# Optimization experiments

Measured on AMD Instinct MI355X. Metric: run time of the kernel, lower is better.

Reference implementation:

```python
import jax, jax.numpy as jnp
import numpy as np
import math

B, N, D, KA, H = 8, 1024, 512, 16, 8
QD = D // 4
HD = D // H


def qsplit(x):
    q = x.shape[-1] // 4
    return x[..., :q], x[..., q:2*q], x[..., 2*q:3*q], x[..., 3*q:]


def hprod(p, q):
    pr, pi, pj, pk = qsplit(p)
    qr, qi, qj, qk = qsplit(q)
    return jnp.concatenate([
        pr*qr - pi*qi - pj*qj - pk*qk,
        pr*qi + pi*qr + pj*qk - pk*qj,
        pr*qj - pi*qk + pj*qr + pk*qi,
        pr*qk + pi*qj - pj*qi + pk*qr,
    ], axis=-1)


def qconj(x):
    r, i, j, k = qsplit(x)
    return jnp.concatenate([r, -i, -j, -k], axis=-1)


def qlin(x, w, b):
    # w: [4, qo, qi] -> Hamilton block matrix [4qo, 4qi]
    r, i, j, k = w[0], w[1], w[2], w[3]
    W = jnp.concatenate([
        jnp.concatenate([r, -i, -j, -k], axis=1),
        jnp.concatenate([i,  r, -k,  j], axis=1),
        jnp.concatenate([j,  k,  r, -i], axis=1),
        jnp.concatenate([k, -j,  i,  r], axis=1),
    ], axis=0)
    return x @ W.T + b


def qln(x, gamma, beta):
    # per-component LayerNorm over Q; gamma/beta: [4, Q]
    qd = x.shape[-1] // 4
    xs = x.reshape(x.shape[:-1] + (4, qd))
    m = xs.mean(-1, keepdims=True)
    v = xs.var(-1, keepdims=True)
    y = (xs - m) / jnp.sqrt(v + 1e-5) * gamma + beta
    return y.reshape(x.shape)


def setup_inputs():
    key = jax.random.key(0)
    ks = jax.random.split(key, 20)
    lim = math.sqrt(6.0 / (2 * QD))  # xavier for [QD, QD]
    def qw(k):
        return jax.random.uniform(k, (4, QD, QD), minval=-lim, maxval=lim)
    return {
        'q': jax.random.normal(ks[0], (B, N, D), dtype=jnp.float32),
        'spike': jax.random.uniform(ks[1], (B, N), dtype=jnp.float32),
        'mask': jnp.ones((B, N), dtype=jnp.float32),
        'theta_logit': jnp.float32(0.0),
        'w_prim': qw(ks[2]), 'b_prim': jnp.zeros((D,), jnp.float32),
        'anchors': jax.random.normal(ks[3], (KA, D)) * 0.5,
        'log_sigma': jnp.zeros((KA,), jnp.float32),
        'w_aggr': qw(ks[4]), 'b_aggr': jnp.zeros((D,), jnp.float32),
        'w_q': qw(ks[5]), 'b_q': jnp.zeros((D,), jnp.float32),
        'w_k': qw(ks[6]), 'b_k': jnp.zeros((D,), jnp.float32),
        'w_v': qw(ks[7]), 'b_v': jnp.zeros((D,), jnp.float32),
        'w_o': qw(ks[8]), 'b_o': jnp.zeros((D,), jnp.float32),
        'ln_gamma': jnp.ones((4, QD), jnp.float32),
        'ln_beta': jnp.zeros((4, QD), jnp.float32),
    }


def reference(q, spike, mask, theta_logit, w_prim, b_prim, anchors, log_sigma,
              w_aggr, b_aggr, w_q, b_q, w_k, b_k, w_v, b_v, w_o, b_o,
              ln_gamma, ln_beta):
    b, n, d = q.shape
    qd = d // 4
    # --- SpikeQuaternionRotation: rotate toward K-axis by theta = theta_max*spike ---
    theta_max = (jnp.pi / 2) * jax.nn.sigmoid(theta_logit)
    theta = theta_max * spike                      # [B, N]
    c = jnp.cos(theta)[..., None]
    s = jnp.sin(theta)[..., None]
    z = jnp.zeros_like(c)
    rot = jnp.concatenate([
        jnp.broadcast_to(c, (b, n, qd)),
        jnp.broadcast_to(z, (b, n, qd)),
        jnp.broadcast_to(z, (b, n, qd)),
        jnp.broadcast_to(s, (b, n, qd)),
    ], axis=-1)
    q_rot = hprod(rot, q)                          # [B, N, D]

    # --- PrimaryLayer: per-cell quaternion transform ---
    msg_p = qlin(q_rot, w_prim, b_prim)

    # --- QuaternionAnchorLayer ---
    a_conj = qconj(anchors)                        # [KA, D]
    prod = hprod(q_rot[:, None, :, :], a_conj[None, :, None, :])  # [B, KA, N, D]
    dist = jnp.sum(prod * prod, axis=-1)           # [B, KA, N]
    sigma_sq = jnp.maximum(jnp.exp(log_sigma) ** 2, 1e-6)
    incid = jnp.exp(-dist / sigma_sq[None, :, None]) * mask[:, None, :]
    denom = jnp.maximum(incid.sum(-1, keepdims=True), 1e-6)
    h = jnp.einsum('bkn,bnd->bkd', incid, q_rot) / denom  # [B, KA, D]
    h = qlin(h, w_aggr, b_aggr)

    # --- QuaternionMHA(query=q_rot, key=h, value=h), no mask ---
    Qh = qlin(q_rot, w_q, b_q).reshape(b, n, H, HD)
    Kh = qlin(h, w_k, b_k).reshape(b, KA, H, HD)
    Vh = qlin(h, w_v, b_v).reshape(b, KA, H, HD)
    scores = jnp.einsum('bqhd,bkhd->bhqk', Qh, Kh) / jnp.sqrt(jnp.float32(HD))
    attn = jax.nn.softmax(scores, axis=-1)
    out = jnp.einsum('bhqk,bkhd->bqhd', attn, Vh).reshape(b, n, d)
    msg_a = qlin(out, w_o, b_o)

    # --- residual + per-component LayerNorm ---
    return qln(q + msg_p + msg_a, ln_gamma, ln_beta)
```

## Files before the change

kernel.cpp:

```cpp
#include <hip/hip_runtime.h>
#include <hip/hip_bf16.h>

typedef __hip_bfloat16 bf16;
typedef __attribute__((ext_vector_type(8))) short bf16x8;
typedef __attribute__((ext_vector_type(4))) float f32x4;

__device__ __forceinline__ float bflo(unsigned u) { return __uint_as_float(u << 16); }
__device__ __forceinline__ float bfhi(unsigned u) { return __uint_as_float(u & 0xffff0000u); }
__device__ __forceinline__ bool probe_f32(const void* mask) {
  return *(const unsigned*)mask == 0x3F800000u;
}
__device__ __forceinline__ float ldin(const void* p, size_t i, bool f32) {
  return f32 ? ((const float*)p)[i] : (float)((const bf16*)p)[i];
}


__global__ __launch_bounds__(256) void prologue(
    const void* w0, const void* w1, const void* w2, const void* w3,
    const void* w4, const void* w5,
    const void* b0, const void* b1, const void* b2, const void* b3,
    const void* b4, const void* b5, const void* g_, const void* be,
    const void* q, const void* spike, const void* theta_logit, const void* mask,
    bf16* __restrict__ Wall, float* __restrict__ biasF,
    bf16* __restrict__ q_rot, float* __restrict__ qn) {
  bool f32 = probe_f32(mask);
  int blk = blockIdx.x, t = threadIdx.x;
  if (blk < 1536) {
    const int compT[4][4] = {{0,1,2,3},{1,0,3,2},{2,3,0,1},{3,2,1,0}};
    const float signT[4][4] = {{1.f,-1.f,-1.f,-1.f},{1.f,1.f,-1.f,1.f},{1.f,1.f,1.f,-1.f},{1.f,-1.f,1.f,1.f}};
    int E = blk * 1024 + t * 4;
    int g = E >> 9;
    int wi = g >> 9;
    int o = g & 511;
    int k0 = E & 511;
    const void* src = wi == 0 ? w0 : wi == 1 ? w1 : wi == 2 ? w2 : wi == 3 ? w3 : wi == 4 ? w4 : w5;
    int ro = o >> 7, a = o & 127, co = k0 >> 7;
    int comp = compT[ro][co];
    float sgn = signT[ro][co];
    bf16 ov[4];
    #pragma unroll
    for (int j = 0; j < 4; ++j) {
      int b2 = (k0 & 127) + j;
      ov[j] = (bf16)(ldin(src, comp * 16384 + a * 128 + b2, f32) * sgn);
    }
    int r = g & 63, c = k0 >> 3;
    size_t off = (size_t)(g >> 6) * 65536 + (size_t)((c >> 2) * 4096 + (r >> 4) * 1024
               + ((c & 3) * 16 + (r & 15)) * 16 + (k0 & 7) * 2);
    *(uint2*)((char*)Wall + off) = *(const uint2*)ov;
  } else if (blk < 1544) {
    int b = blk - 1536;
    const void* src = b == 0 ? b0 : b == 1 ? b1 : b == 2 ? b2 : b == 3 ? b3
                    : b == 4 ? b4 : b == 5 ? b5 : b == 6 ? g_ : be;
    biasF[b * 512 + t] = ldin(src, t, f32);
    biasF[b * 512 + 256 + t] = ldin(src, 256 + t, f32);
  } else {
    int row = (blk - 1544) * 2 + (t >> 7);
    int l = t & 127;
    float tl = ldin(theta_logit, 0, f32);
    float tmax = 1.5707963267948966f / (1.0f + __expf(-tl));
    float th = tmax * ldin(spike, row, f32);
    float c = cosf(th), s = sinf(th);
    size_t base = (size_t)row * 512;
    float a = ldin(q, base + l, f32), b = ldin(q, base + 128 + l, f32);
    float cc = ldin(q, base + 256 + l, f32), d = ldin(q, base + 384 + l, f32);
    float r0 = c * a - s * d;
    float r1 = c * b - s * cc;
    float r2 = c * cc + s * b;
    float r3 = c * d + s * a;
    bf16* orow = q_rot + base;
    orow[l] = (bf16)r0; orow[128 + l] = (bf16)r1; orow[256 + l] = (bf16)r2; orow[384 + l] = (bf16)r3;
    qn[(size_t)row * 128 + l] = r0 * r0 + r1 * r1 + r2 * r2 + r3 * r3;
  }
}

__device__ __forceinline__ void stage_B64(const bf16* __restrict__ Bw, int n0, char* Bs, int t) {
  const char* src = (const char*)Bw + (size_t)(n0 >> 6) * 65536;
  #pragma unroll
  for (int i = 0; i < 16; ++i)
    *(uint4*)(Bs + t * 16 + i * 4096) = *(const uint4*)(src + t * 16 + i * 4096);
}

__global__ __launch_bounds__(256, 2) void gemm_dist(
    const bf16* __restrict__ A, const bf16* __restrict__ Bw,
    const float* __restrict__ bias0, const float* __restrict__ bias1,
    bf16* __restrict__ MQ,
    const float* __restrict__ qn, const void* anchors, const void* lsig,
    const void* mask, float* __restrict__ h_part, float* __restrict__ pd_part) {
  __shared__ char smem[77952];
  const int t = threadIdx.x;
  if (blockIdx.x >= 128) {
    char* Bs = smem;
    const int g = blockIdx.x - 128;
    const int wave = t >> 6, lane = t & 63;
    const int quad = lane >> 4, l16 = lane & 15;
    const int m0 = (g & 31) * 256, n0 = (g >> 5) * 64;
    stage_B64(Bw, n0, Bs, t);
    __syncthreads();
    const int mbase = m0 + wave * 64;
    f32x4 acc[4][4] = {};
    bf16x8 areg[2][4], breg[2][4];
    #pragma unroll
    for (int mt = 0; mt < 4; ++mt)
      areg[0][mt] = *(const bf16x8*)(A + (size_t)(mbase + mt * 16 + l16) * 512 + quad * 8);
    #pragma unroll
    for (int nt = 0; nt < 4; ++nt)
      breg[0][nt] = *(const bf16x8*)(Bs + nt * 1024 + lane * 16);
    #pragma unroll
    for (int kk = 0; kk < 16; ++kk) {
      const int cur = kk & 1, nxt = cur ^ 1;
      if (kk < 15) {
        const int k2 = (kk + 1) * 32;
        #pragma unroll
        for (int mt = 0; mt < 4; ++mt)
          areg[nxt][mt] = *(const bf16x8*)(A + (size_t)(mbase + mt * 16 + l16) * 512 + k2 + quad * 8);
        #pragma unroll
        for (int nt = 0; nt < 4; ++nt)
          breg[nxt][nt] = *(const bf16x8*)(Bs + (kk + 1) * 4096 + nt * 1024 + lane * 16);
      }
      #pragma unroll
      for (int mt = 0; mt < 4; ++mt)
        #pragma unroll
        for (int nt = 0; nt < 4; ++nt)
          acc[mt][nt] = __builtin_amdgcn_mfma_f32_16x16x32_bf16(areg[cur][mt], breg[cur][nt],
                                                                acc[mt][nt], 0, 0, 0);
    }
    #pragma unroll
    for (int nt = 0; nt < 4; ++nt) {
      int col = n0 + nt * 16 + l16;
      float bv = col < 512 ? bias0[col] : bias1[col - 512];
      #pragma unroll
      for (int mt = 0; mt < 4; ++mt) {
        int rb = mbase + mt * 16 + quad * 4;
        #pragma unroll
        for (int r = 0; r < 4; ++r)
          MQ[(size_t)(rb + r) * 1024 + col] = (bf16)(acc[mt][nt][r] + bv);
      }
    }
  } else {
    bool f32 = probe_f32(mask);
    bf16*  qr   = (bf16*)smem;
    float* an   = (float*)(smem + 65536);
    float* sInc = (float*)(smem + 73728);
    float* rs   = (float*)(smem + 77824);
    float* pd   = (float*)(smem + 77888);
    int bb = blockIdx.x;
    int b = bb >> 4, nc = bb & 15;
    {
      const uint4* src = (const uint4*)((const bf16*)A + ((size_t)b * 1024 + nc * 64) * 512);
      uint4* dst = (uint4*)qr;
      #pragma unroll
      for (int i = 0; i < 16; ++i) dst[t + i * 256] = src[t + i * 256];
    }
    for (int i = t; i < 2048; i += 256) {
      int k = i >> 7, l = i & 127;
      float a0 = ldin(anchors, k * 512 + l, f32);
      float a1 = ldin(anchors, k * 512 + 128 + l, f32);
      float a2 = ldin(anchors, k * 512 + 256 + l, f32);
      float a3 = ldin(anchors, k * 512 + 384 + l, f32);
      an[i] = a0 * a0 + a1 * a1 + a2 * a2 + a3 * a3;
    }
    if (t < 16) {
      float ls = ldin(lsig, t, f32);
      float ssq = __expf(ls); ssq = fmaxf(ssq * ssq, 1e-6f);
      rs[t] = -1.0f / ssq;
      pd[t] = 0.0f;
    }
    __syncthreads();
    {
      int rl = t >> 2, part = t & 3;
      int n = nc * 64 + rl;
      const float* qrow = qn + ((size_t)b * 1024 + n) * 128 + part * 32;
      f32x4 q4[8];
      #pragma unroll
      for (int i = 0; i < 8; ++i) q4[i] = *(const f32x4*)(qrow + i * 4);
      float sc[16] = {};
      #pragma unroll
      for (int i = 0; i < 8; ++i) {
        #pragma unroll
        for (int k = 0; k < 16; ++k) {
          f32x4 av = *(const f32x4*)(an + k * 128 + part * 32 + i * 4);
          sc[k] += q4[i][0] * av[0] + q4[i][1] * av[1] + q4[i][2] * av[2] + q4[i][3] * av[3];
        }
      }
      #pragma unroll
      for (int k = 0; k < 16; ++k) {
        sc[k] += __shfl_xor(sc[k], 1, 64);
        sc[k] += __shfl_xor(sc[k], 2, 64);
      }
      if (part == 0) {
        float mval = ldin(mask, b * 1024 + n, f32);
        #pragma unroll
        for (int k = 0; k < 16; ++k) {
          float inc = __expf(sc[k] * rs[k]) * mval;
          sInc[k * 64 + rl] = inc;
          atomicAdd(&pd[k], inc);
        }
      }
    }
    __syncthreads();
    {
      float acc0[16] = {}, acc1[16] = {};
      for (int nn = 0; nn < 64; ++nn) {
        float v0 = (float)qr[nn * 512 + t];
        float v1 = (float)qr[nn * 512 + 256 + t];
        #pragma unroll
        for (int k = 0; k < 16; ++k) {
          float p = sInc[k * 64 + nn];
          acc0[k] += p * v0;
          acc1[k] += p * v1;
        }
      }
      #pragma unroll
      for (int k = 0; k < 16; ++k) {
        size_t base = ((size_t)(b * 16 + k) * 16 + nc) * 512;
        h_part[base + t] = acc0[k];
        h_part[base + 256 + t] = acc1[k];
      }
    }
    if (t < 16) pd_part[((size_t)(b * 16 + t)) * 16 + nc] = pd[t];
  }
}

__device__ __forceinline__ float dotW(const char* WallB, int gRow, const float* xp512) {
  const char* p = WallB + (size_t)(gRow >> 6) * 65536
                + (size_t)(((gRow >> 4) & 3) * 1024 + (gRow & 15) * 16);
  float acc = 0.0f;
  #pragma unroll 4
  for (int c4 = 0; c4 < 16; ++c4) {
    #pragma unroll
    for (int cl = 0; cl < 4; ++cl) {
      uint4 u = *(const uint4*)(p + c4 * 4096 + cl * 256);
      const float* xp = xp512 + c4 * 32 + cl * 8;
      acc += xp[0] * bflo(u.x) + xp[1] * bfhi(u.x)
           + xp[2] * bflo(u.y) + xp[3] * bfhi(u.y)
           + xp[4] * bflo(u.z) + xp[5] * bfhi(u.z)
           + xp[6] * bflo(u.w) + xp[7] * bfhi(u.w);
    }
  }
  return acc;
}

__global__ __launch_bounds__(256) void qlin_akv(
    const float* __restrict__ h_part, const float* __restrict__ pd_part,
    const bf16* __restrict__ Wall, const float* __restrict__ biasF,
    float* __restrict__ Kh, float* __restrict__ Vh) {
  __shared__ float xs[512];
  __shared__ float ys[512];
  const char* WallB = (const char*)Wall;
  const float* ba = biasF + 1536;
  const float* bk = biasF + 2048;
  const float* bv = biasF + 2560;
  int row = blockIdx.x, half = blockIdx.y;
  int t = threadIdx.x;
  float dsum = 0.0f;
  #pragma unroll
  for (int nc = 0; nc < 16; ++nc) dsum += pd_part[row * 16 + nc];
  float dinv = 1.0f / fmaxf(dsum, 1e-6f);
  #pragma unroll
  for (int j = 0; j < 2; ++j) {
    int d = j * 256 + t;
    float hv = 0.0f;
    #pragma unroll
    for (int nc = 0; nc < 16; ++nc) hv += h_part[(size_t)row * 8192 + nc * 512 + d];
    xs[d] = hv * dinv;
  }
  __syncthreads();
  #pragma unroll
  for (int j = 0; j < 2; ++j) {
    int o = j * 256 + t;
    ys[o] = ba[o] + dotW(WallB, 1536 + o, xs);
  }
  __syncthreads();
  {
    int o = half * 256 + t;
    float ak = bk[o] + dotW(WallB, 2048 + o, ys);
    float av = bv[o] + dotW(WallB, 2560 + o, ys);
    Kh[(size_t)row * 512 + o] = ak;
    Vh[(size_t)row * 512 + o] = av;
  }
}

__global__ __launch_bounds__(256, 2) void attn_tail(
    const bf16* __restrict__ MQ, const float* __restrict__ Kh_g,
    const float* __restrict__ Vh_g, const bf16* __restrict__ Wall,
    const float* __restrict__ biasF, const void* q, const void* mask, void* out) {
  __shared__ float KV[8 * 1092];
  __shared__ float P[16 * 132];
  const bool f32 = probe_f32(mask);
  const int t = threadIdx.x;
  const int rowbase = blockIdx.x * 16;
  const int b = rowbase >> 10;
  for (int i = t; i < 8192; i += 256) {
    int k = i >> 9, d = i & 511, h = d >> 6, dd = d & 63;
    KV[h * 1092 + k * 68 + dd] = Kh_g[(size_t)b * 8192 + i];
  }
  __syncthreads();
  {
    const int r = t >> 4, h = (t >> 1) & 7, hf = t & 1;
    const int grow = rowbase + r;
    const uint4* qp = (const uint4*)(MQ + (size_t)grow * 1024 + 512 + h * 64 + hf * 32);
    float qv[32];
    #pragma unroll
    for (int i = 0; i < 4; ++i) {
      uint4 u = qp[i];
      qv[i * 8 + 0] = bflo(u.x); qv[i * 8 + 1] = bfhi(u.x);
      qv[i * 8 + 2] = bflo(u.y); qv[i * 8 + 3] = bfhi(u.y);
      qv[i * 8 + 4] = bflo(u.z); qv[i * 8 + 5] = bfhi(u.z);
      qv[i * 8 + 6] = bflo(u.w); qv[i * 8 + 7] = bfhi(u.w);
    }
    float sc[16];
    #pragma unroll
    for (int k = 0; k < 16; ++k) {
      float s = 0.0f;
      #pragma unroll
      for (int d4 = 0; d4 < 8; ++d4) {
        f32x4 kv = *(const f32x4*)(KV + h * 1092 + k * 68 + hf * 32 + d4 * 4);
        s += qv[d4 * 4 + 0] * kv[0] + qv[d4 * 4 + 1] * kv[1]
           + qv[d4 * 4 + 2] * kv[2] + qv[d4 * 4 + 3] * kv[3];
      }
      sc[k] = s;
    }
    #pragma unroll
    for (int k = 0; k < 16; ++k) sc[k] += __shfl_xor(sc[k], 1, 64);
    if (hf == 0) {
      #pragma unroll
      for (int k = 0; k < 16; ++k) sc[k] *= 0.125f;
      float m = sc[0];
      #pragma unroll
      for (int k = 1; k < 16; ++k) m = fmaxf(m, sc[k]);
      float ssum = 0.0f;
      #pragma unroll
      for (int k = 0; k < 16; ++k) { sc[k] = __expf(sc[k] - m); ssum += sc[k]; }
      float inv = 1.0f / ssum;
      #pragma unroll
      for (int k = 0; k < 16; ++k) P[r * 132 + h * 16 + k] = sc[k] * inv;
    }
  }
  __syncthreads();
  for (int i = t; i < 8192; i += 256) {
    int k = i >> 9, d = i & 511, h = d >> 6, dd = d & 63;
    KV[h * 1092 + k * 68 + dd] = Vh_g[(size_t)b * 8192 + i];
  }
  __syncthreads();
  float pv[8][4];
  {
    const int r = t >> 4, dg = t & 15;
    #pragma unroll
    for (int h = 0; h < 8; ++h) {
      float a0 = 0, a1 = 0, a2 = 0, a3 = 0;
      #pragma unroll
      for (int k = 0; k < 16; ++k) {
        float p = P[r * 132 + h * 16 + k];
        f32x4 va = *(const f32x4*)(KV + h * 1092 + k * 68 + dg * 4);
        a0 += p * va[0]; a1 += p * va[1]; a2 += p * va[2]; a3 += p * va[3];
      }
      pv[h][0] = a0; pv[h][1] = a1; pv[h][2] = a2; pv[h][3] = a3;
    }
  }
  __syncthreads();
  char* A_lds = (char*)KV;
  {
    const int r = t >> 4, dg = t & 15;
    #pragma unroll
    for (int h = 0; h < 8; ++h) {
      int c0 = h * 64 + dg * 4;
      int off = (c0 >> 5) * 1024 + ((c0 >> 3) & 3) * 256 + r * 16 + (c0 & 7) * 2;
      bf16 ov[4] = {(bf16)pv[h][0], (bf16)pv[h][1], (bf16)pv[h][2], (bf16)pv[h][3]};
      *(uint2*)(A_lds + off) = *(const uint2*)ov;
    }
  }
  __syncthreads();
  const int wave = t >> 6, lane = t & 63, quad = lane >> 4, l16 = lane & 15;
  const char* WallB = (const char*)Wall;
  f32x4 acc[8] = {};
  bf16x8 breg[2][8];
  bf16x8 areg[2];
  areg[0] = *(const bf16x8*)(A_lds + quad * 256 + l16 * 16);
  #pragma unroll
  for (int nt = 0; nt < 8; ++nt) {
    size_t cb = (size_t)(16 + wave * 2 + (nt >> 2)) * 65536;
    breg[0][nt] = *(const bf16x8*)(WallB + cb + (nt & 3) * 1024 + lane * 16);
  }
  #pragma unroll
  for (int kk = 0; kk < 16; ++kk) {
    const int cur = kk & 1, nxt = cur ^ 1;
    if (kk < 15) {
      areg[nxt] = *(const bf16x8*)(A_lds + (kk + 1) * 1024 + quad * 256 + l16 * 16);
      #pragma unroll
      for (int nt = 0; nt < 8; ++nt) {
        size_t cb = (size_t)(16 + wave * 2 + (nt >> 2)) * 65536;
        breg[nxt][nt] = *(const bf16x8*)(WallB + cb + (kk + 1) * 4096 + (nt & 3) * 1024 + lane * 16);
      }
    }
    #pragma unroll
    for (int nt = 0; nt < 8; ++nt)
      acc[nt] = __builtin_amdgcn_mfma_f32_16x16x32_bf16(areg[cur], breg[cur][nt], acc[nt], 0, 0, 0);
  }
  const float* biasO = biasF + 1024;
  const float* gamF = biasF + 3072;
  float xv[8][4];
  float s[4] = {0, 0, 0, 0}, s2[4] = {0, 0, 0, 0};
  #pragma unroll
  for (int nt = 0; nt < 8; ++nt) {
    int gcol = wave * 128 + nt * 16 + l16;
    float bo = biasO[gcol];
    #pragma unroll
    for (int reg = 0; reg < 4; ++reg) {
      int grow = rowbase + quad * 4 + reg;
      float qv = ldin(q, (size_t)grow * 512 + gcol, f32);
      float mp = (float)MQ[(size_t)grow * 1024 + gcol];
      float x = qv + mp + acc[nt][reg] + bo;
      xv[nt][reg] = x;
      s[reg] += x; s2[reg] += x * x;
    }
  }
  #pragma unroll
  for (int reg = 0; reg < 4; ++reg) {
    #pragma unroll
    for (int off = 1; off <= 8; off <<= 1) {
      s[reg]  += __shfl_xor(s[reg], off, 64);
      s2[reg] += __shfl_xor(s2[reg], off, 64);
    }
  }
  #pragma unroll
  for (int reg = 0; reg < 4; ++reg) {
    float m = s[reg] * (1.0f / 128.0f);
    float rinv = rsqrtf(s2[reg] * (1.0f / 128.0f) - m * m + 1e-5f);
    int grow = rowbase + quad * 4 + reg;
    #pragma unroll
    for (int nt = 0; nt < 8; ++nt) {
      int gcol = wave * 128 + nt * 16 + l16;
      float y = (xv[nt][reg] - m) * rinv * gamF[gcol] + gamF[512 + gcol];
      if (f32) ((float*)out)[(size_t)grow * 512 + gcol] = y;
      else     ((bf16*)out)[(size_t)grow * 512 + gcol] = (bf16)y;
    }
  }
}

extern "C" void kernel_launch(void* const* d_in, const int* in_sizes, int n_in,
                              void* d_out, int out_size, void* d_ws, size_t ws_size,
                              hipStream_t stream) {
  (void)in_sizes; (void)n_in; (void)out_size; (void)ws_size;
  const void* q      = d_in[0];
  const void* spike  = d_in[1];
  const void* mask   = d_in[2];
  const void* tl     = d_in[3];
  const void* w_prim = d_in[4];
  const void* b_prim = d_in[5];
  const void* anchors= d_in[6];
  const void* lsig   = d_in[7];
  const void* w_aggr = d_in[8];
  const void* b_aggr = d_in[9];
  const void* w_q    = d_in[10];
  const void* b_q    = d_in[11];
  const void* w_k    = d_in[12];
  const void* b_k    = d_in[13];
  const void* w_v    = d_in[14];
  const void* b_v    = d_in[15];
  const void* w_o    = d_in[16];
  const void* b_o    = d_in[17];
  const void* gam    = d_in[18];
  const void* bet    = d_in[19];

  char* ws = (char*)d_ws;
  bf16*  Wall   = (bf16*)(ws + 0);
  bf16*  q_rot  = (bf16*)(ws + 3145728);
  float* qn     = (float*)(ws + 11534336);
  bf16*  MQ     = (bf16*)(ws + 15728640);
  float* h_part = (float*)(ws + 32505856);
  float* pd_part= (float*)(ws + 36700160);
  float* Kh     = (float*)(ws + 36708352);
  float* Vh     = (float*)(ws + 36970496);
  float* biasF  = (float*)(ws + 37232640);

  prologue<<<5640, 256, 0, stream>>>(w_prim, w_q, w_o, w_aggr, w_k, w_v,
                                     b_prim, b_q, b_o, b_aggr, b_k, b_v, gam, bet,
                                     q, spike, tl, mask, Wall, biasF, q_rot, qn);
  gemm_dist<<<640, 256, 0, stream>>>(q_rot, Wall, biasF + 0, biasF + 512, MQ,
                                     qn, anchors, lsig, mask, h_part, pd_part);
  qlin_akv<<<dim3(128, 2), 256, 0, stream>>>(h_part, pd_part, Wall, biasF, Kh, Vh);
  attn_tail<<<512, 256, 0, stream>>>(MQ, Kh, Vh, Wall, biasF, q, mask, d_out);
}
```

Measured before the change: 227.8 us.

## Split aggregation and K/V projection into two wider-grid kernels with split-K reductions

Replaces the single 256-block qlin_akv kernel, in which each thread ran a full 512-long dot product serially, with two kernels of 1024 blocks each. The first computes the aggregation projection and the second the K and V projections. Each output row is now split across four lanes, each covering a quarter of the input, and the partials are combined with wave shuffles. This removes the redundant per-block recomputation of the aggregation layer and exposes far more parallelism for this latency-bound stage. The cost is an extra kernel launch, a global round trip through a new h_aggr buffer, and the h_part reduction being recomputed in 8 blocks per row.

```diff
diff --git a/kernel.cpp b/kernel.cpp
--- a/kernel.cpp
+++ b/kernel.cpp
@@ -221,12 +221,12 @@
   }
 }
 
-__device__ __forceinline__ float dotW(const char* WallB, int gRow, const float* xp512) {
+__device__ __forceinline__ float dotW4(const char* WallB, int gRow, const float* xp512, int c4lo) {
   const char* p = WallB + (size_t)(gRow >> 6) * 65536
                 + (size_t)(((gRow >> 4) & 3) * 1024 + (gRow & 15) * 16);
   float acc = 0.0f;
-  #pragma unroll 4
-  for (int c4 = 0; c4 < 16; ++c4) {
+  #pragma unroll
+  for (int c4 = c4lo; c4 < c4lo + 4; ++c4) {
     #pragma unroll
     for (int cl = 0; cl < 4; ++cl) {
       uint4 u = *(const uint4*)(p + c4 * 4096 + cl * 256);
@@ -240,18 +240,15 @@
   return acc;
 }
 
-__global__ __launch_bounds__(256) void qlin_akv(
+__global__ __launch_bounds__(256) void aggr_k(
     const float* __restrict__ h_part, const float* __restrict__ pd_part,
     const bf16* __restrict__ Wall, const float* __restrict__ biasF,
-    float* __restrict__ Kh, float* __restrict__ Vh) {
+    float* __restrict__ h_aggr) {
   __shared__ float xs[512];
-  __shared__ float ys[512];
   const char* WallB = (const char*)Wall;
   const float* ba = biasF + 1536;
-  const float* bk = biasF + 2048;
-  const float* bv = biasF + 2560;
-  int row = blockIdx.x, half = blockIdx.y;
-  int t = threadIdx.x;
+  const int gy = blockIdx.x >> 7, row = blockIdx.x & 127;
+  const int t = threadIdx.x;
   float dsum = 0.0f;
   #pragma unroll
   for (int nc = 0; nc < 16; ++nc) dsum += pd_part[row * 16 + nc];
@@ -265,18 +262,39 @@
     xs[d] = hv * dinv;
   }
   __syncthreads();
+  const int o = gy * 64 + (t >> 2), part = t & 3;
+  float acc = dotW4(WallB, 1536 + o, xs, part * 4);
+  acc += __shfl_xor(acc, 1, 64);
+  acc += __shfl_xor(acc, 2, 64);
+  if (part == 0) h_aggr[(size_t)row * 512 + o] = acc + ba[o];
+}
+
+__global__ __launch_bounds__(256) void kv_k(
+    const float* __restrict__ h_aggr, const bf16* __restrict__ Wall,
+    const float* __restrict__ biasF,
+    float* __restrict__ Kh, float* __restrict__ Vh) {
+  __shared__ float ys[512];
+  const char* WallB = (const char*)Wall;
+  const float* bk = biasF + 2048;
+  const float* bv = biasF + 2560;
+  const int gy = blockIdx.x >> 7, row = blockIdx.x & 127;
+  const int t = threadIdx.x;
   #pragma unroll
   for (int j = 0; j < 2; ++j) {
-    int o = j * 256 + t;
-    ys[o] = ba[o] + dotW(WallB, 1536 + o, xs);
-  }
-  __syncthreads();
-  {
-    int o = half * 256 + t;
-    float ak = bk[o] + dotW(WallB, 2048 + o, ys);
-    float av = bv[o] + dotW(WallB, 2560 + o, ys);
-    Kh[(size_t)row * 512 + o] = ak;
-    Vh[(size_t)row * 512 + o] = av;
+    int d = j * 256 + t;
+    ys[d] = h_aggr[(size_t)row * 512 + d];
+  }
+  __syncthreads();
+  const int o = gy * 64 + (t >> 2), part = t & 3;
+  float ak = dotW4(WallB, 2048 + o, ys, part * 4);
+  float av = dotW4(WallB, 2560 + o, ys, part * 4);
+  ak += __shfl_xor(ak, 1, 64);
+  ak += __shfl_xor(ak, 2, 64);
+  av += __shfl_xor(av, 1, 64);
+  av += __shfl_xor(av, 2, 64);
+  if (part == 0) {
+    Kh[(size_t)row * 512 + o] = ak + bk[o];
+    Vh[(size_t)row * 512 + o] = av + bv[o];
   }
 }
 
@@ -472,12 +490,14 @@
   float* Kh     = (float*)(ws + 36708352);
   float* Vh     = (float*)(ws + 36970496);
   float* biasF  = (float*)(ws + 37232640);
+  float* h_aggr = (float*)(ws + 37249024);
 
   prologue<<<5640, 256, 0, stream>>>(w_prim, w_q, w_o, w_aggr, w_k, w_v,
                                      b_prim, b_q, b_o, b_aggr, b_k, b_v, gam, bet,
                                      q, spike, tl, mask, Wall, biasF, q_rot, qn);
   gemm_dist<<<640, 256, 0, stream>>>(q_rot, Wall, biasF + 0, biasF + 512, MQ,
                                      qn, anchors, lsig, mask, h_part, pd_part);
-  qlin_akv<<<dim3(128, 2), 256, 0, stream>>>(h_part, pd_part, Wall, biasF, Kh, Vh);
+  aggr_k<<<1024, 256, 0, stream>>>(h_part, pd_part, Wall, biasF, h_aggr);
+  kv_k<<<1024, 256, 0, stream>>>(h_aggr, Wall, biasF, Kh, Vh);
   attn_tail<<<512, 256, 0, stream>>>(MQ, Kh, Vh, Wall, biasF, q, mask, d_out);
 }
```

Result: faster. 195.5 us (-14.2%).
